# Performance work log

Hardware: AMD Instinct MI355X
Metric: run time of the kernel (lower is better)

Reference implementation:

```python
import jax, jax.numpy as jnp
import numpy as np


def setup_inputs() -> dict:
    key = jax.random.key(0)
    k1, k2, k3, k4, k5 = jax.random.split(key, 5)
    S, B, He, Hd, A = 2048, 32, 1024, 1024, 512
    dec_out = jax.random.normal(k1, (B, Hd), dtype=jnp.float32)
    enc_outs = jax.random.normal(k2, (S, B, He), dtype=jnp.float32)
    # parameter scales matching nn.Linear default init (~U(-1/sqrt(fan_in), ...))
    W_enc = jax.random.normal(k3, (A, He), dtype=jnp.float32) / np.sqrt(He)
    W_dec = jax.random.normal(k4, (A, Hd), dtype=jnp.float32) / np.sqrt(Hd)
    att_v = jax.random.normal(k5, (A,), dtype=jnp.float32) / np.sqrt(A)
    return {"dec_out": dec_out, "enc_outs": enc_outs, "W_enc": W_enc,
            "W_dec": W_dec, "att_v": att_v}


def reference(dec_out, enc_outs, W_enc, W_dec, att_v):
    # enc_att: (S, B, A) = enc_outs @ W_enc^T
    enc_att = jnp.einsum('sbh,ah->sba', enc_outs, W_enc)
    # dec_att: (B, A) = dec_out @ W_dec^T, tiled over seq_len
    dec_att = jnp.einsum('bh,ah->ba', dec_out, W_dec)
    # additive score: tanh(enc_att + dec_att) . att_v  -> (B, S)
    dec_enc_att = jnp.tanh(enc_att + dec_att[None, :, :])      # (S, B, A)
    scores = jnp.einsum('sba,a->bs', dec_enc_att, att_v)       # (B, S)
    weights = jax.nn.softmax(scores, axis=-1)                  # (B, S)
    # context: weighted sum of encoder outputs -> (B, He)
    context = jnp.einsum('bs,sbh->bh', weights, enc_outs)
    return context, weights
```

## Files before the change

### kernel.cpp

```cpp
#include <hip/hip_runtime.h>
#include <hip/hip_bf16.h>


typedef float f32x4 __attribute__((ext_vector_type(4)));
typedef __bf16 bf16x8 __attribute__((ext_vector_type(8)));

#define WS_DEC_OFF    0u
#define WS_WIMG_OFF   65536u
#define WS_SCORES_OFF (65536u + 1048576u)
#define WS_PART_OFF   (65536u + 1048576u + 262144u)

__device__ __forceinline__ void gload_lds16(const void* g, void* l) {
  __builtin_amdgcn_global_load_lds(
      (const __attribute__((address_space(1))) void*)g,
      (__attribute__((address_space(3))) void*)l, 16, 0, 0);
}

__global__ void dec_att_kernel(const float* __restrict__ dec_out,
                               const float* __restrict__ W_dec,
                               float* __restrict__ out) {
  int gtid = blockIdx.x * blockDim.x + threadIdx.x;
  int w = gtid >> 6;
  int lane = gtid & 63;
  int b = w >> 9;
  int a = w & 511;
  const float4* dp = (const float4*)(dec_out + b * 1024);
  const float4* wp = (const float4*)(W_dec + a * 1024);
  float sum = 0.f;
#pragma unroll
  for (int i = 0; i < 4; ++i) {
    float4 x = dp[lane + i * 64];
    float4 y = wp[lane + i * 64];
    sum += x.x * y.x + x.y * y.y + x.z * y.z + x.w * y.w;
  }
#pragma unroll
  for (int m = 32; m; m >>= 1) sum += __shfl_xor(sum, m, 64);
  if (lane == 0) out[b * 512 + a] = sum;
}

__global__ void convert_wenc(const float* __restrict__ W, __bf16* __restrict__ out) {
  int idx = blockIdx.x * 256 + threadIdx.x;
  int kc = idx >> 14;
  int q = (idx >> 12) & 3;
  int row = (idx >> 3) & 511;
  int j = idx & 7;
  out[idx] = (__bf16)W[row * 1024 + kc * 32 + q * 8 + j];
}

__global__ __launch_bounds__(256, 2) void scores_gemm(
    const float* __restrict__ enc,
    const __bf16* __restrict__ wimg,
    const float* __restrict__ dec_att,
    const float* __restrict__ attv,
    float* __restrict__ scores) {
  __shared__ __align__(16) char smem[73728];
  float (*part)[4] = (float(*)[4])smem;

  const int tid = threadIdx.x;
  const int lane = tid & 63;
  const int wc = tid >> 6;
  const int q = lane >> 4;
  const int c0 = lane & 15;
  const int bm = blockIdx.x;

  f32x4 acc[4][8];
#pragma unroll
  for (int i = 0; i < 4; ++i)
#pragma unroll
    for (int j = 0; j < 8; ++j) acc[i][j] = (f32x4){0.f, 0.f, 0.f, 0.f};

  const int srow = tid >> 2;
  const int sq = tid & 3;
  const float* asrc = enc + (size_t)(bm * 64 + srow) * 1024 + sq * 8;
  const char* bimg = (const char*)wimg;
  const int a_woff = sq * 1024 + srow * 16;

  {
    const float4* as4 = (const float4*)asrc;
    float4 x = as4[0], y = as4[1];
#pragma unroll
    for (int p = 0; p < 8; ++p)
      gload_lds16(bimg + p * 4096 + tid * 16, smem + 8192 + p * 4096 + tid * 16);
    bf16x8 v;
    v[0] = (__bf16)x.x; v[1] = (__bf16)x.y; v[2] = (__bf16)x.z; v[3] = (__bf16)x.w;
    v[4] = (__bf16)y.x; v[5] = (__bf16)y.y; v[6] = (__bf16)y.z; v[7] = (__bf16)y.w;
    *(bf16x8*)(smem + a_woff) = v;
  }
  __syncthreads();

  for (int t = 0; t < 32; ++t) {
    const int cur = t & 1;
    char* ab = smem + cur * 4096;
    char* bb = smem + 8192 + cur * 32768;
    float4 an0, an1;
    if (t < 31) {
      const char* bs = bimg + (size_t)(t + 1) * 32768;
      char* bd = smem + 8192 + (cur ^ 1) * 32768;
#pragma unroll
      for (int p = 0; p < 8; ++p)
        gload_lds16(bs + p * 4096 + tid * 16, bd + p * 4096 + tid * 16);
      const float4* as4 = (const float4*)(asrc + (t + 1) * 32);
      an0 = as4[0]; an1 = as4[1];
    }
    bf16x8 af[4], bfr[8];
#pragma unroll
    for (int mf = 0; mf < 4; ++mf)
      af[mf] = *(const bf16x8*)(ab + q * 1024 + (mf * 16 + c0) * 16);
#pragma unroll
    for (int nf = 0; nf < 8; ++nf)
      bfr[nf] = *(const bf16x8*)(bb + q * 8192 + (wc * 128 + nf * 16 + c0) * 16);
    __builtin_amdgcn_s_setprio(1);
#pragma unroll
    for (int mf = 0; mf < 4; ++mf)
#pragma unroll
      for (int nf = 0; nf < 8; ++nf)
        acc[mf][nf] = __builtin_amdgcn_mfma_f32_16x16x32_bf16(af[mf], bfr[nf],
                                                              acc[mf][nf], 0, 0, 0);
    __builtin_amdgcn_s_setprio(0);
    if (t < 31) {
      bf16x8 v;
      v[0] = (__bf16)an0.x; v[1] = (__bf16)an0.y; v[2] = (__bf16)an0.z; v[3] = (__bf16)an0.w;
      v[4] = (__bf16)an1.x; v[5] = (__bf16)an1.y; v[6] = (__bf16)an1.z; v[7] = (__bf16)an1.w;
      *(bf16x8*)(smem + (cur ^ 1) * 4096 + a_woff) = v;
    }
    __syncthreads();
  }

  float av[8];
#pragma unroll
  for (int nf = 0; nf < 8; ++nf) av[nf] = attv[wc * 128 + nf * 16 + c0];

#pragma unroll
  for (int mf = 0; mf < 4; ++mf) {
#pragma unroll
    for (int rg = 0; rg < 4; ++rg) {
      const int rl = mf * 16 + q * 4 + rg;
      const int b = rl & 31;
      const float* drow = dec_att + b * 512 + wc * 128 + c0;
      float sum = 0.f;
#pragma unroll
      for (int nf = 0; nf < 8; ++nf) {
        float x = acc[mf][nf][rg] + drow[nf * 16];
        float e = __expf(2.f * x);
        float t = 1.f - 2.f / (e + 1.f);
        sum += t * av[nf];
      }
      sum += __shfl_xor(sum, 1, 64);
      sum += __shfl_xor(sum, 2, 64);
      sum += __shfl_xor(sum, 4, 64);
      sum += __shfl_xor(sum, 8, 64);
      if (c0 == 0) part[rl][wc] = sum;
    }
  }
  __syncthreads();
  if (tid < 64) {
    float tot = part[tid][0] + part[tid][1] + part[tid][2] + part[tid][3];
    int r = bm * 64 + tid;
    scores[(r & 31) * 2048 + (r >> 5)] = tot;
  }
}

__global__ void softmax_kernel(const float* __restrict__ scores,
                               float* __restrict__ weights) {
  const int b = blockIdx.x;
  const int t = threadIdx.x;
  const float4* row = (const float4*)(scores + b * 2048);
  float4 v0 = row[t];
  float4 v1 = row[t + 256];
  float m = fmaxf(fmaxf(fmaxf(v0.x, v0.y), fmaxf(v0.z, v0.w)),
                  fmaxf(fmaxf(v1.x, v1.y), fmaxf(v1.z, v1.w)));
#pragma unroll
  for (int s = 32; s; s >>= 1) m = fmaxf(m, __shfl_xor(m, s, 64));
  __shared__ float redm[4], reds[4];
  if ((t & 63) == 0) redm[t >> 6] = m;
  __syncthreads();
  m = fmaxf(fmaxf(redm[0], redm[1]), fmaxf(redm[2], redm[3]));
  float4 e0, e1;
  e0.x = __expf(v0.x - m); e0.y = __expf(v0.y - m);
  e0.z = __expf(v0.z - m); e0.w = __expf(v0.w - m);
  e1.x = __expf(v1.x - m); e1.y = __expf(v1.y - m);
  e1.z = __expf(v1.z - m); e1.w = __expf(v1.w - m);
  float s8 = e0.x + e0.y + e0.z + e0.w + e1.x + e1.y + e1.z + e1.w;
#pragma unroll
  for (int s = 32; s; s >>= 1) s8 += __shfl_xor(s8, s, 64);
  if ((t & 63) == 0) reds[t >> 6] = s8;
  __syncthreads();
  float inv = 1.f / (reds[0] + reds[1] + reds[2] + reds[3]);
  e0.x *= inv; e0.y *= inv; e0.z *= inv; e0.w *= inv;
  e1.x *= inv; e1.y *= inv; e1.z *= inv; e1.w *= inv;
  float4* wrow = (float4*)(weights + b * 2048);
  wrow[t] = e0;
  wrow[t + 256] = e1;
}

__global__ void ctx_partial(const float* __restrict__ enc,
                            const float* __restrict__ weights,
                            float* __restrict__ part) {
  const int bid = blockIdx.x;
  const int t = threadIdx.x;
  const int b = bid & 31;
  const int hc = (bid >> 5) & 3;
  const int sc = bid >> 7;
  const int h = hc * 256 + t;
  const float* wrow = weights + b * 2048 + sc * 128;
  const float* ebase = enc + ((size_t)(sc * 128) * 32 + b) * 1024 + h;
  float acc = 0.f;
#pragma unroll 4
  for (int i = 0; i < 128; ++i) acc += wrow[i] * ebase[(size_t)i * 32768];
  part[(size_t)(sc * 32 + b) * 1024 + h] = acc;
}

__global__ void ctx_reduce(const float* __restrict__ part, float* __restrict__ ctx) {
  int idx = blockIdx.x * 256 + threadIdx.x;
  float s = 0.f;
#pragma unroll
  for (int c = 0; c < 16; ++c) s += part[c * 32768 + idx];
  ctx[idx] = s;
}

extern "C" void kernel_launch(void* const* d_in, const int* in_sizes, int n_in,
                              void* d_out, int out_size, void* d_ws, size_t ws_size,
                              hipStream_t stream) {
  const float* dec_out  = (const float*)d_in[0];
  const float* enc_outs = (const float*)d_in[1];
  const float* W_enc    = (const float*)d_in[2];
  const float* W_dec    = (const float*)d_in[3];
  const float* att_v    = (const float*)d_in[4];

  float* out = (float*)d_out;
  float* ctx = out;
  float* weights = out + 32768;

  char* ws = (char*)d_ws;
  float*  ws_dec    = (float*)(ws + WS_DEC_OFF);
  __bf16* ws_wimg   = (__bf16*)(ws + WS_WIMG_OFF);
  float*  ws_scores = (float*)(ws + WS_SCORES_OFF);
  float*  ws_part   = (float*)(ws + WS_PART_OFF);

  dec_att_kernel<<<4096, 256, 0, stream>>>(dec_out, W_dec, ws_dec);
  convert_wenc<<<2048, 256, 0, stream>>>(W_enc, ws_wimg);
  scores_gemm<<<1024, 256, 0, stream>>>(enc_outs, ws_wimg, ws_dec, att_v, ws_scores);
  softmax_kernel<<<32, 256, 0, stream>>>(ws_scores, weights);
  ctx_partial<<<2048, 256, 0, stream>>>(enc_outs, weights, ws_part);
  ctx_reduce<<<128, 256, 0, stream>>>(ws_part, ctx);
}
```

Before: 159.3 us.

## Change LDS tile layout, use manual waitcnt barriers, vectorize context partial

The bf16 weight image and the A tile in LDS switch from a quarter-interleaved layout to row-major rows of 64 bytes, so each thread writes its converted A chunk contiguously and reads fragments through precomputed offsets. The __syncthreads calls in the GEMM loop become explicit s_waitcnt vmcnt/lgkmcnt plus s_barrier, which lets the next tile's loads stay in flight across the barrier. ctx_partial now loads float4 per thread and launches a quarter as many blocks, cutting per-block index overhead. The 64-byte row stride may cause more LDS bank conflicts on fragment reads, and the hand-counted vmcnt must match the number of outstanding loads.

```diff
diff --git a/kernel.cpp b/kernel.cpp
--- a/kernel.cpp
+++ b/kernel.cpp
@@ -9,6 +9,11 @@
 #define WS_WIMG_OFF   65536u
 #define WS_SCORES_OFF (65536u + 1048576u)
 #define WS_PART_OFF   (65536u + 1048576u + 262144u)
+
+#define WAITVM10()  asm volatile("s_waitcnt vmcnt(10)" ::: "memory")
+#define WAITVM0()   asm volatile("s_waitcnt vmcnt(0)" ::: "memory")
+#define WAITLGKM0() asm volatile("s_waitcnt lgkmcnt(0)" ::: "memory")
+#define SBAR()      asm volatile("s_barrier" ::: "memory")
 
 __device__ __forceinline__ void gload_lds16(const void* g, void* l) {
   __builtin_amdgcn_global_load_lds(
@@ -41,10 +46,9 @@
 __global__ void convert_wenc(const float* __restrict__ W, __bf16* __restrict__ out) {
   int idx = blockIdx.x * 256 + threadIdx.x;
   int kc = idx >> 14;
-  int q = (idx >> 12) & 3;
-  int row = (idx >> 3) & 511;
-  int j = idx & 7;
-  out[idx] = (__bf16)W[row * 1024 + kc * 32 + q * 8 + j];
+  int row = (idx >> 5) & 511;
+  int j = idx & 31;
+  out[idx] = (__bf16)W[row * 1024 + kc * 32 + j];
 }
 
 __global__ __launch_bounds__(256, 2) void scores_gemm(
@@ -73,7 +77,12 @@
   const int sq = tid & 3;
   const float* asrc = enc + (size_t)(bm * 64 + srow) * 1024 + sq * 8;
   const char* bimg = (const char*)wimg;
-  const int a_woff = sq * 1024 + srow * 16;
+
+  int a_roff[4], b_roff[8];
+#pragma unroll
+  for (int mf = 0; mf < 4; ++mf) a_roff[mf] = (mf * 16 + c0) * 64 + q * 16;
+#pragma unroll
+  for (int nf = 0; nf < 8; ++nf) b_roff[nf] = (wc * 128 + nf * 16 + c0) * 64 + q * 16;
 
   {
     const float4* as4 = (const float4*)asrc;
@@ -84,9 +93,9 @@
     bf16x8 v;
     v[0] = (__bf16)x.x; v[1] = (__bf16)x.y; v[2] = (__bf16)x.z; v[3] = (__bf16)x.w;
     v[4] = (__bf16)y.x; v[5] = (__bf16)y.y; v[6] = (__bf16)y.z; v[7] = (__bf16)y.w;
-    *(bf16x8*)(smem + a_woff) = v;
-  }
-  __syncthreads();
+    *(bf16x8*)(smem + tid * 16) = v;
+    WAITLGKM0();
+  }
 
   for (int t = 0; t < 32; ++t) {
     const int cur = t & 1;
@@ -94,21 +103,23 @@
     char* bb = smem + 8192 + cur * 32768;
     float4 an0, an1;
     if (t < 31) {
+      const float4* as4 = (const float4*)(asrc + (t + 1) * 32);
+      an0 = as4[0]; an1 = as4[1];
       const char* bs = bimg + (size_t)(t + 1) * 32768;
       char* bd = smem + 8192 + (cur ^ 1) * 32768;
 #pragma unroll
       for (int p = 0; p < 8; ++p)
         gload_lds16(bs + p * 4096 + tid * 16, bd + p * 4096 + tid * 16);
-      const float4* as4 = (const float4*)(asrc + (t + 1) * 32);
-      an0 = as4[0]; an1 = as4[1];
+      WAITVM10();
+    } else {
+      WAITVM0();
     }
+    SBAR();
     bf16x8 af[4], bfr[8];
 #pragma unroll
-    for (int mf = 0; mf < 4; ++mf)
-      af[mf] = *(const bf16x8*)(ab + q * 1024 + (mf * 16 + c0) * 16);
-#pragma unroll
-    for (int nf = 0; nf < 8; ++nf)
-      bfr[nf] = *(const bf16x8*)(bb + q * 8192 + (wc * 128 + nf * 16 + c0) * 16);
+    for (int mf = 0; mf < 4; ++mf) af[mf] = *(const bf16x8*)(ab + a_roff[mf]);
+#pragma unroll
+    for (int nf = 0; nf < 8; ++nf) bfr[nf] = *(const bf16x8*)(bb + b_roff[nf]);
     __builtin_amdgcn_s_setprio(1);
 #pragma unroll
     for (int mf = 0; mf < 4; ++mf)
@@ -121,9 +132,10 @@
       bf16x8 v;
       v[0] = (__bf16)an0.x; v[1] = (__bf16)an0.y; v[2] = (__bf16)an0.z; v[3] = (__bf16)an0.w;
       v[4] = (__bf16)an1.x; v[5] = (__bf16)an1.y; v[6] = (__bf16)an1.z; v[7] = (__bf16)an1.w;
-      *(bf16x8*)(smem + (cur ^ 1) * 4096 + a_woff) = v;
+      *(bf16x8*)(smem + (cur ^ 1) * 4096 + tid * 16) = v;
     }
-    __syncthreads();
+    WAITLGKM0();
+    SBAR();
   }
 
   float av[8];
@@ -196,18 +208,19 @@
 __global__ void ctx_partial(const float* __restrict__ enc,
                             const float* __restrict__ weights,
                             float* __restrict__ part) {
-  const int bid = blockIdx.x;
+  const int b = blockIdx.x & 31;
+  const int sc = blockIdx.x >> 5;
   const int t = threadIdx.x;
-  const int b = bid & 31;
-  const int hc = (bid >> 5) & 3;
-  const int sc = bid >> 7;
-  const int h = hc * 256 + t;
   const float* wrow = weights + b * 2048 + sc * 128;
-  const float* ebase = enc + ((size_t)(sc * 128) * 32 + b) * 1024 + h;
-  float acc = 0.f;
+  const char* ebase = (const char*)(enc + ((size_t)(sc * 128) * 32 + b) * 1024) + t * 16;
+  float4 acc = {0.f, 0.f, 0.f, 0.f};
 #pragma unroll 4
-  for (int i = 0; i < 128; ++i) acc += wrow[i] * ebase[(size_t)i * 32768];
-  part[(size_t)(sc * 32 + b) * 1024 + h] = acc;
+  for (int i = 0; i < 128; ++i) {
+    float4 e = *(const float4*)(ebase + (size_t)i * 131072);
+    float ws = wrow[i];
+    acc.x += ws * e.x; acc.y += ws * e.y; acc.z += ws * e.z; acc.w += ws * e.w;
+  }
+  *(float4*)(part + (size_t)(sc * 32 + b) * 1024 + t * 4) = acc;
 }
 
 __global__ void ctx_reduce(const float* __restrict__ part, float* __restrict__ ctx) {
@@ -241,6 +254,6 @@
   convert_wenc<<<2048, 256, 0, stream>>>(W_enc, ws_wimg);
   scores_gemm<<<1024, 256, 0, stream>>>(enc_outs, ws_wimg, ws_dec, att_v, ws_scores);
   softmax_kernel<<<32, 256, 0, stream>>>(ws_scores, weights);
-  ctx_partial<<<2048, 256, 0, stream>>>(enc_outs, weights, ws_part);
+  ctx_partial<<<512, 256, 0, stream>>>(enc_outs, weights, ws_part);
   ctx_reduce<<<128, 256, 0, stream>>>(ws_part, ctx);
 }
```

After: 184.2 us. 1.16x slower.
